# Performance work log

Measured on AMD Instinct MI355X. Metric: run time of the kernel, lower is better.

## Reference

```python
import jax, jax.numpy as jnp
import numpy as np

D = 1024; DI = 2048; HS = 16; PS = DI // HS; NS = 64; KC = 4; CHUNK = 64
HA = 16; HKV = 4; PA = D // HA; MLP_MULT = 4; ROPE_BASE = 10000.0
B_SZ = 2; L_SEQ = 2048


def rms_norm(x):
    eps = jnp.asarray(jnp.finfo(x.dtype).eps, x.dtype)
    return x * jax.lax.rsqrt(jnp.mean(jnp.square(x), axis=-1, keepdims=True) + eps)


def silu(x):
    return x * jax.nn.sigmoid(x)


def apply_rope(x, cos, sin):
    half = x.shape[-1] // 2
    x1, x2 = x[..., :half], x[..., half:]
    return jnp.concatenate([x1 * cos + x2 * sin, -x1 * sin + x2 * cos], axis=-1)


def selective_scan(x, A, Bm, Cm, dt, chunk):
    # x: [B,L,H,P], Bm/Cm: [B,L,H,N], A/dt: [H]. L must be a multiple of chunk.
    Bb, L, H, P = x.shape
    N = Bm.shape[-1]
    decay = jnp.exp(A * dt)  # [H]
    nc = L // chunk
    xp = x.reshape(Bb, nc, chunk, H, P).transpose(0, 1, 3, 2, 4)   # [B,nc,H,cs,P]
    Bp = Bm.reshape(Bb, nc, chunk, H, N).transpose(0, 1, 3, 2, 4)  # [B,nc,H,cs,N]
    Cp = Cm.reshape(Bb, nc, chunk, H, N).transpose(0, 1, 3, 2, 4)
    x_dt = xp * dt[None, None, :, None, None]
    idx = jnp.arange(chunk)
    diff = idx[:, None] - idx[None, :]
    # intra-chunk causal decay matrix L_mat: [H,cs,cs]
    Lm = jnp.where(diff >= 0, decay[:, None, None] ** jnp.maximum(diff, 0), 0.0)
    CB = jnp.einsum('bchqn,bchkn->bchqk', Cp, Bp)
    y_diag = jnp.einsum('bchqk,bchkp->bchqp', CB * Lm[None, None], x_dt)
    # per-chunk states
    decay_rev = decay[:, None] ** (chunk - 1 - idx)[None, :]  # [H,cs]
    states = jnp.einsum('bchtn,bchtp->bchnp', Bp * decay_rev[None, None, :, :, None], x_dt)
    # inter-chunk propagation
    ci = jnp.arange(nc)
    shift = ci[:, None] - ci[None, :] - 1
    cdec = decay ** chunk
    M = jnp.where(shift >= 0, cdec[:, None, None] ** jnp.maximum(shift, 0), 0.0)  # [H,nc,nc]
    h_carry = jnp.einsum('hij,bjhnp->bihnp', M, states)
    decay_out = decay[:, None] ** (idx + 1)[None, :]  # [H,cs]
    y_off = jnp.einsum('bchtn,bchnp->bchtp', Cp, h_carry) * decay_out[None, None, :, :, None]
    y = (y_diag + y_off).transpose(0, 1, 3, 2, 4).reshape(Bb, L, H, P)
    return y


def mlp(n, fc_w, proj_w):
    h = jax.nn.relu(n @ fc_w)
    return jnp.square(h) @ proj_w


def setup_inputs() -> dict:
    key = jax.random.key(0)
    ks = jax.random.split(key, 24)
    w = lambda k, shp, s=0.02: jax.random.normal(k, shp, jnp.float32) * s
    dt_init = jax.random.uniform(ks[0], (HS,), jnp.float32, 0.001, 0.1)
    dt_bias = dt_init + jnp.log(-jnp.expm1(-dt_init))  # inverse softplus
    return {
        'x': jax.random.normal(ks[1], (B_SZ, L_SEQ, D), jnp.float32),
        'in_proj_w': w(ks[2], (D, 2 * DI)),
        'conv_w': w(ks[3], (DI, KC), 0.2),
        'conv_b': jnp.zeros((DI,), jnp.float32),
        'B_proj_w': w(ks[4], (D, HS * NS)),
        'C_proj_w': w(ks[5], (D, HS * NS)),
        'dt_bias': dt_bias,
        'A_log': jnp.log(jnp.arange(1, HS + 1, dtype=jnp.float32)),
        'D_param': jnp.ones((HS,), jnp.float32),
        'out_proj_w': w(ks[6], (DI, D)),
        'resid_mix_m': jnp.stack([jnp.ones(D), jnp.zeros(D)]).astype(jnp.float32),
        'mamba_scale': jnp.ones((D,), jnp.float32),
        'm_fc_w': w(ks[7], (D, MLP_MULT * D)),
        'm_proj_w': w(ks[8], (MLP_MULT * D, D)),
        'm_mlp_scale': jnp.ones((D,), jnp.float32),
        'resid_mix_a': jnp.stack([jnp.ones(D), jnp.zeros(D)]).astype(jnp.float32),
        'q_w': w(ks[9], (D, D)),
        'k_w': w(ks[10], (D, HKV * PA)),
        'v_w': w(ks[11], (D, HKV * PA)),
        'o_w': w(ks[12], (D, D)),
        'q_gain': jnp.full((HA,), 1.0, jnp.float32),
        'attn_scale': jnp.ones((D,), jnp.float32),
        'a_fc_w': w(ks[13], (D, MLP_MULT * D)),
        'a_proj_w': w(ks[14], (MLP_MULT * D, D)),
        'a_mlp_scale': jnp.ones((D,), jnp.float32),
    }


def reference(x, in_proj_w, conv_w, conv_b, B_proj_w, C_proj_w, dt_bias, A_log, D_param, out_proj_w, resid_mix_m, mamba_scale, m_fc_w, m_proj_w, m_mlp_scale, resid_mix_a, q_w, k_w, v_w, o_w, q_gain, attn_scale, a_fc_w, a_proj_w, a_mlp_scale):
    Bb, L, _ = x.shape
    x0 = x
    # ---- Mamba block ----
    xm = resid_mix_m[0][None, None] * x + resid_mix_m[1][None, None] * x0
    n = rms_norm(xm)
    vg = n @ in_proj_w
    value, gate = vg[..., :DI], vg[..., DI:]
    v_t = value.transpose(0, 2, 1)  # [B, DI, L]
    v_conv = jax.lax.conv_general_dilated(
        v_t, conv_w[:, None, :], (1,), [(KC - 1, 0)],
        feature_group_count=DI, dimension_numbers=('NCH', 'OIH', 'NCH')) + conv_b[None, :, None]
    value = silu(v_conv).transpose(0, 2, 1).reshape(Bb, L, HS, PS)
    Bm = (xm @ B_proj_w).reshape(Bb, L, HS, NS)  # B/C use pre-norm (mixed) input
    Cm = (xm @ C_proj_w).reshape(Bb, L, HS, NS)
    dt = jax.nn.softplus(dt_bias)
    A = -jnp.exp(A_log)
    y = selective_scan(value, A, Bm, Cm, dt, CHUNK)
    y = y + D_param[None, None, :, None] * value
    y = (y.reshape(Bb, L, DI) * silu(gate)) @ out_proj_w
    xm = xm + mamba_scale[None, None] * y
    xm = xm + m_mlp_scale[None, None] * mlp(rms_norm(xm), m_fc_w, m_proj_w)
    # ---- Attention block ----
    xa = resid_mix_a[0][None, None] * xm + resid_mix_a[1][None, None] * x0
    n = rms_norm(xa)
    q = (n @ q_w).reshape(Bb, L, HA, PA).transpose(0, 2, 1, 3)
    k = (n @ k_w).reshape(Bb, L, HKV, PA).transpose(0, 2, 1, 3)
    v = (n @ v_w).reshape(Bb, L, HKV, PA).transpose(0, 2, 1, 3)
    q = rms_norm(q); k = rms_norm(k)
    inv_freq = 1.0 / (ROPE_BASE ** (jnp.arange(0, PA, 2, dtype=jnp.float32) / PA))
    f = jnp.outer(jnp.arange(L, dtype=jnp.float32), inv_freq)
    cos, sin = jnp.cos(f)[None, None], jnp.sin(f)[None, None]
    q = apply_rope(q, cos, sin) * q_gain[None, :, None, None]
    k = apply_rope(k, cos, sin)
    G = HA // HKV
    k = jnp.repeat(k, G, axis=1); v = jnp.repeat(v, G, axis=1)
    s = jnp.einsum('bhqd,bhkd->bhqk', q, k) / np.float32(np.sqrt(PA))
    mask = jnp.tril(jnp.ones((L, L), bool))
    s = jnp.where(mask[None, None], s, jnp.asarray(-jnp.inf, s.dtype))
    att = jax.nn.softmax(s, axis=-1)
    y = jnp.einsum('bhqk,bhkd->bhqd', att, v).transpose(0, 2, 1, 3).reshape(Bb, L, D)
    xa = xa + attn_scale[None, None] * (y @ o_w)
    xa = xa + a_mlp_scale[None, None] * mlp(rms_norm(xa), a_fc_w, a_proj_w)
    return xa
```

## Files before the change

### kernel.cpp

```cpp
#include <hip/hip_runtime.h>
#include <hip/hip_bf16.h>
#include <math.h>

#define D_ 1024
#define DI_ 2048
#define HS_ 16
#define PS_ 128
#define NS_ 64
#define HA_ 16
#define HKV_ 4
#define PA_ 64
#define B_ 2
#define L_ 2048
#define NT_ 4096
#define NC_ 32
#define RMS_EPS_ 1.1920929e-7f

typedef __attribute__((ext_vector_type(8))) short short8;
typedef __attribute__((ext_vector_type(4))) float f32x4;

#define GLOAD_LDS16(gp, lp)                                                        \
  __builtin_amdgcn_global_load_lds(                                               \
      (const __attribute__((address_space(1))) unsigned int*)(gp),                \
      (__attribute__((address_space(3))) unsigned int*)(lp), 16, 0, 0)

__global__ __launch_bounds__(256) void transpose_cvt(
    const float* __restrict__ W, __hip_bfloat16* __restrict__ Wt, int K, int N, int ldw) {
  __shared__ float t[32][33];
  int n0 = blockIdx.x * 32, k0 = blockIdx.y * 32;
  int tx = threadIdx.x & 31, ty = threadIdx.x >> 5;
#pragma unroll
  for (int i = 0; i < 4; i++)
    t[ty + i * 8][tx] = W[(size_t)(k0 + ty + i * 8) * ldw + n0 + tx];
  __syncthreads();
#pragma unroll
  for (int i = 0; i < 4; i++)
    Wt[(size_t)(n0 + ty + i * 8) * K + k0 + tx] = __float2bfloat16(t[tx][ty + i * 8]);
}

template<int BN>
__global__ __launch_bounds__(256) void gemm_bf16_t(
    const unsigned short* __restrict__ A, const unsigned short* __restrict__ Wt,
    float* __restrict__ Cf, __hip_bfloat16* __restrict__ Cb,
    const float* __restrict__ baseb, const float* __restrict__ scale,
    int N, int K, int gn, int mode) {
  constexpr int nWc = BN / 64;
  constexpr int nWr = 4 / nWc;
  constexpr int MF  = 8 / nWr;
  __shared__ unsigned short As[2][128 * 64];
  __shared__ unsigned short Bs[2][BN * 64];
  int lid = blockIdx.x;
  int x = lid & 7, r = lid >> 3;
  int RN = gn >> 2;
  int bm = ((x >> 2) * 16 + (r & 15)) * 128;
  int bn = ((x & 3) * RN + (r >> 4)) * BN;
  int tid = threadIdx.x;
  int w = tid >> 6, l = tid & 63;
  int wr = w / nWc, wc = w % nWc;
  int l15 = l & 15, lg = l >> 4;
  f32x4 acc[MF][4];
#pragma unroll
  for (int i = 0; i < MF; i++)
#pragma unroll
    for (int j = 0; j < 4; j++) acc[i][j] = (f32x4){0.f, 0.f, 0.f, 0.f};
  int r_ = tid >> 3;
  int s_ = tid & 7;

  auto STAGE = [&](int k0, int nb) {
#pragma unroll
    for (int i = 0; i < 4; i++) {
      int rr = i * 32 + r_;
      int kq = s_ ^ (rr & 7);
      GLOAD_LDS16(A + (size_t)(bm + rr) * K + k0 + kq * 8, &As[nb][rr * 64 + s_ * 8]);
    }
#pragma unroll
    for (int i = 0; i < BN / 32; i++) {
      int rr = i * 32 + r_;
      int kq = s_ ^ (rr & 7);
      GLOAD_LDS16(Wt + (size_t)(bn + rr) * K + k0 + kq * 8, &Bs[nb][rr * 64 + s_ * 8]);
    }
  };

  STAGE(0, 0);
  __syncthreads();
  int cur = 0;
  for (int k0 = 0; k0 < K; k0 += 64) {
    if (k0 + 64 < K) STAGE(k0 + 64, cur ^ 1);
#pragma unroll
    for (int h = 0; h < 2; h++) {
      short8 af[MF], bfr[4];
#pragma unroll
      for (int i = 0; i < MF; i++) {
        int row = wr * (16 * MF) + i * 16 + l15;
        int c = h * 4 + lg;
        af[i] = *(const short8*)&As[cur][row * 64 + ((c ^ (row & 7)) << 3)];
      }
#pragma unroll
      for (int j = 0; j < 4; j++) {
        int row = wc * 64 + j * 16 + l15;
        int c = h * 4 + lg;
        bfr[j] = *(const short8*)&Bs[cur][row * 64 + ((c ^ (row & 7)) << 3)];
      }
#pragma unroll
      for (int i = 0; i < MF; i++)
#pragma unroll
        for (int j = 0; j < 4; j++)
          acc[i][j] = __builtin_amdgcn_mfma_f32_16x16x32_bf16(af[i], bfr[j], acc[i][j], 0, 0, 0);
    }
    __syncthreads();
    cur ^= 1;
  }
  int rb = lg * 4, cb2 = l15;
#pragma unroll
  for (int i = 0; i < MF; i++)
#pragma unroll
    for (int j = 0; j < 4; j++) {
      int gr = bm + wr * (16 * MF) + i * 16 + rb;
      int gc = bn + wc * 64 + j * 16 + cb2;
#pragma unroll
      for (int reg = 0; reg < 4; reg++) {
        float v = acc[i][j][reg];
        size_t idx = (size_t)(gr + reg) * N + gc;
        if (mode == 0) {
          Cf[idx] = v;
        } else if (mode == 1) {
          v = fmaxf(v, 0.f);
          Cb[idx] = __float2bfloat16(v * v);
        } else if (mode == 2) {
          Cb[idx] = __float2bfloat16(v);
        } else {
          Cf[idx] = baseb[idx] + scale[gc] * v;
        }
      }
    }
}

__global__ __launch_bounds__(256) void mix_rms_kernel(
    const float* __restrict__ a, const float* __restrict__ b2,
    const float* __restrict__ mix, float* __restrict__ xout,
    __hip_bfloat16* __restrict__ nbf, __hip_bfloat16* __restrict__ rawbf) {
  int row = blockIdx.x;
  size_t base = (size_t)row * D_;
  float v[4]; float ss = 0.f;
#pragma unroll
  for (int i = 0; i < 4; i++) {
    int d = threadIdx.x + i * 256;
    float val = mix[d] * a[base + d] + mix[D_ + d] * b2[base + d];
    v[i] = val; ss += val * val;
  }
  for (int o = 32; o > 0; o >>= 1) ss += __shfl_down(ss, o, 64);
  __shared__ float red[4];
  if ((threadIdx.x & 63) == 0) red[threadIdx.x >> 6] = ss;
  __syncthreads();
  float inv = rsqrtf((red[0] + red[1] + red[2] + red[3]) * (1.f / D_) + RMS_EPS_);
#pragma unroll
  for (int i = 0; i < 4; i++) {
    int d = threadIdx.x + i * 256;
    xout[base + d] = v[i];
    nbf[base + d] = __float2bfloat16(v[i] * inv);
    if (rawbf) rawbf[base + d] = __float2bfloat16(v[i]);
  }
}

__global__ __launch_bounds__(256) void rms_kernel(
    const float* __restrict__ a, __hip_bfloat16* __restrict__ nbf) {
  int row = blockIdx.x;
  size_t base = (size_t)row * D_;
  float v[4]; float ss = 0.f;
#pragma unroll
  for (int i = 0; i < 4; i++) {
    int d = threadIdx.x + i * 256;
    float val = a[base + d];
    v[i] = val; ss += val * val;
  }
  for (int o = 32; o > 0; o >>= 1) ss += __shfl_down(ss, o, 64);
  __shared__ float red[4];
  if ((threadIdx.x & 63) == 0) red[threadIdx.x >> 6] = ss;
  __syncthreads();
  float inv = rsqrtf((red[0] + red[1] + red[2] + red[3]) * (1.f / D_) + RMS_EPS_);
#pragma unroll
  for (int i = 0; i < 4; i++) {
    int d = threadIdx.x + i * 256;
    nbf[base + d] = __float2bfloat16(v[i] * inv);
  }
}

__global__ __launch_bounds__(256) void conv_silu_kernel(
    const __hip_bfloat16* __restrict__ vg, const float* __restrict__ cw,
    const float* __restrict__ cb, float* __restrict__ xv) {
  int idx = blockIdx.x * 256 + threadIdx.x;
  int c = idx & (DI_ - 1);
  int bl = idx >> 11;
  int l = bl & (L_ - 1);
  float acc = cb[c];
  float w0 = cw[c * 4 + 0], w1 = cw[c * 4 + 1], w2 = cw[c * 4 + 2], w3 = cw[c * 4 + 3];
  size_t rb = (size_t)bl * 4096 + c;
  if (l >= 3) acc += __bfloat162float(vg[rb - (size_t)3 * 4096]) * w0;
  if (l >= 2) acc += __bfloat162float(vg[rb - (size_t)2 * 4096]) * w1;
  if (l >= 1) acc += __bfloat162float(vg[rb - (size_t)1 * 4096]) * w2;
  acc += __bfloat162float(vg[rb]) * w3;
  xv[idx] = acc / (1.f + __expf(-acc));
}

__global__ __launch_bounds__(256) void scanA1_kernel(
    const float* __restrict__ xv, const __hip_bfloat16* __restrict__ BCm,
    const float* __restrict__ dt_bias, const float* __restrict__ A_log,
    float* __restrict__ st) {
  __shared__ __align__(16) float sm[4096 + 8192];
  float* Bs = sm;
  float* Xs = sm + 4096;
  int blk = blockIdx.x;
  int c = blk & 31, h = (blk >> 5) & 15, b = blk >> 9;
  float dt = log1pf(__expf(dt_bias[h]));
  float adt = -__expf(A_log[h]) * dt;
  int tid = threadIdx.x;
  int l0 = c * 64;
  size_t rB = ((size_t)(b * L_ + l0)) * 2048 + h * NS_;
#pragma unroll
  for (int i = 0; i < 16; i++) {
    int e = tid + i * 256;
    int t = e >> 6, n = e & 63;
    Bs[t * 64 + n] = __bfloat162float(BCm[rB + (size_t)t * 2048 + n]);
  }
  size_t rX = ((size_t)(b * L_ + l0)) * DI_ + h * PS_;
#pragma unroll
  for (int i = 0; i < 32; i++) {
    int e = tid + i * 256;
    int t = e >> 7, p = e & 127;
    Xs[t * 128 + p] = xv[rX + (size_t)t * DI_ + p];
  }
  __syncthreads();
  int pg = tid & 31;
  int ng = (tid >> 5) << 3;
  float acc[8][4];
#pragma unroll
  for (int nn = 0; nn < 8; nn++)
#pragma unroll
    for (int i = 0; i < 4; i++) acc[nn][i] = 0.f;
  for (int t = 0; t < 64; t++) {
    float dr = __expf(adt * (float)(63 - t));
    float4 x4 = *(const float4*)&Xs[t * 128 + pg * 4];
    float xd0 = x4.x * dr, xd1 = x4.y * dr, xd2 = x4.z * dr, xd3 = x4.w * dr;
#pragma unroll
    for (int nn = 0; nn < 8; nn++) {
      float bv = Bs[t * 64 + ng + nn];
      acc[nn][0] += bv * xd0; acc[nn][1] += bv * xd1;
      acc[nn][2] += bv * xd2; acc[nn][3] += bv * xd3;
    }
  }
  size_t sb = ((size_t)((b * HS_ + h) * NC_ + c)) * (NS_ * PS_);
#pragma unroll
  for (int nn = 0; nn < 8; nn++) {
    *(float4*)&st[sb + (size_t)(ng + nn) * PS_ + pg * 4] =
        make_float4(acc[nn][0] * dt, acc[nn][1] * dt, acc[nn][2] * dt, acc[nn][3] * dt);
  }
}

__global__ __launch_bounds__(256) void scanA2_kernel(
    const float* __restrict__ xv, const __hip_bfloat16* __restrict__ BCm,
    const float* __restrict__ dt_bias,
    const float* __restrict__ A_log, const float* __restrict__ D_param,
    float* __restrict__ y) {
  __shared__ __align__(16) float sm[4160 + 8192];
  float* Cb = sm;
  float* Bs = sm + 4160;
  float* Xs = sm + 4160;
  int blk = blockIdx.x;
  int c = blk & 31, h = (blk >> 5) & 15, b = blk >> 9;
  float dt = log1pf(__expf(dt_bias[h]));
  float adt = -__expf(A_log[h]) * dt;
  float Dp = D_param[h];
  int tid = threadIdx.x;
  int l0 = c * 64;
  size_t rB = ((size_t)(b * L_ + l0)) * 2048 + h * NS_;
#pragma unroll
  for (int i = 0; i < 16; i++) {
    int e = tid + i * 256;
    int t = e >> 6, n = e & 63;
    Bs[t * 64 + n] = __bfloat162float(BCm[rB + (size_t)t * 2048 + n]);
    Cb[t * 65 + n] = __bfloat162float(BCm[rB + 1024 + (size_t)t * 2048 + n]);
  }
  __syncthreads();
  int q = tid >> 2;
  int kb = (tid & 3) << 4;
  float cbl[16];
#pragma unroll
  for (int kk = 0; kk < 16; kk++) {
    int k = kb + kk;
    float a = 0.f;
    if (k <= q) {
      for (int n = 0; n < 64; n++) a += Cb[q * 65 + n] * Bs[k * 64 + n];
      a *= __expf(adt * (float)(q - k));
    }
    cbl[kk] = a;
  }
  __syncthreads();
#pragma unroll
  for (int kk = 0; kk < 16; kk++) Cb[q * 65 + kb + kk] = cbl[kk];
  size_t rX = ((size_t)(b * L_ + l0)) * DI_ + h * PS_;
#pragma unroll
  for (int i = 0; i < 32; i++) {
    int e = tid + i * 256;
    int t = e >> 7, p = e & 127;
    Xs[t * 128 + p] = xv[rX + (size_t)t * DI_ + p];
  }
  __syncthreads();
  int pg = tid & 31;
  int qg = (tid >> 5) << 3;
  float acc[8][4];
#pragma unroll
  for (int qq = 0; qq < 8; qq++)
#pragma unroll
    for (int i = 0; i < 4; i++) acc[qq][i] = 0.f;
  for (int k = 0; k < 64; k++) {
    float4 x4 = *(const float4*)&Xs[k * 128 + pg * 4];
#pragma unroll
    for (int qq = 0; qq < 8; qq++) {
      float s = Cb[(qg + qq) * 65 + k];
      acc[qq][0] += s * x4.x; acc[qq][1] += s * x4.y;
      acc[qq][2] += s * x4.z; acc[qq][3] += s * x4.w;
    }
  }
#pragma unroll
  for (int qq = 0; qq < 8; qq++) {
    int qr = qg + qq;
    float4 xq = *(const float4*)&Xs[qr * 128 + pg * 4];
    size_t yo = ((size_t)(b * L_ + l0 + qr)) * DI_ + h * PS_ + pg * 4;
    *(float4*)&y[yo] = make_float4(acc[qq][0] * dt + Dp * xq.x,
                                   acc[qq][1] * dt + Dp * xq.y,
                                   acc[qq][2] * dt + Dp * xq.z,
                                   acc[qq][3] * dt + Dp * xq.w);
  }
}

__global__ __launch_bounds__(256) void scanB1_kernel(
    float* __restrict__ st, const float* __restrict__ dt_bias,
    const float* __restrict__ A_log) {
  int slice = blockIdx.x & 3;
  int h = (blockIdx.x >> 2) & 15, b = blockIdx.x >> 6;
  float dt = log1pf(__expf(dt_bias[h]));
  float adt = -__expf(A_log[h]) * dt;
  float cdec = __expf(adt * 64.f);
  size_t base = ((size_t)(b * HS_ + h)) * NC_ * (NS_ * PS_) + slice * 2048 + threadIdx.x;
  float hreg[8];
#pragma unroll
  for (int j = 0; j < 8; j++) hreg[j] = 0.f;
  for (int c = 0; c < NC_; c++) {
    size_t o = base + (size_t)c * (NS_ * PS_);
#pragma unroll
    for (int j = 0; j < 8; j++) {
      float tmp = st[o + (size_t)j * 256];
      st[o + (size_t)j * 256] = hreg[j];
      hreg[j] = cdec * hreg[j] + tmp;
    }
  }
}

__global__ __launch_bounds__(256) void scanB2_kernel(
    const __hip_bfloat16* __restrict__ BCm, const float* __restrict__ st,
    const __hip_bfloat16* __restrict__ vg, const float* __restrict__ dt_bias,
    const float* __restrict__ A_log, const float* __restrict__ y,
    __hip_bfloat16* __restrict__ yout) {
  __shared__ float Cs[64 * 64];
  __shared__ __align__(16) float Hs[64 * 128];
  int blk = blockIdx.x;
  int c = blk & 31, h = (blk >> 5) & 15, b = blk >> 9;
  float dt = log1pf(__expf(dt_bias[h]));
  float adt = -__expf(A_log[h]) * dt;
  int tid = threadIdx.x;
  int l0 = c * 64;
  size_t rC = ((size_t)(b * L_ + l0)) * 2048 + 1024 + h * NS_;
#pragma unroll
  for (int i = 0; i < 16; i++) {
    int e = tid + i * 256;
    int t = e >> 6, n = e & 63;
    Cs[t * 64 + n] = __bfloat162float(BCm[rC + (size_t)t * 2048 + n]);
  }
  size_t sb = ((size_t)((b * HS_ + h) * NC_ + c)) * (NS_ * PS_);
#pragma unroll
  for (int i = 0; i < 32; i++) {
    int e = tid + i * 256;
    Hs[e] = st[sb + e];
  }
  __syncthreads();
  int pg = tid & 31;
  int tg = (tid >> 5) << 3;
  float acc[8][4];
#pragma unroll
  for (int tt = 0; tt < 8; tt++)
#pragma unroll
    for (int i = 0; i < 4; i++) acc[tt][i] = 0.f;
  for (int n = 0; n < 64; n++) {
    float4 h4 = *(const float4*)&Hs[n * 128 + pg * 4];
#pragma unroll
    for (int tt = 0; tt < 8; tt++) {
      float cv = Cs[(tg + tt) * 64 + n];
      acc[tt][0] += cv * h4.x; acc[tt][1] += cv * h4.y;
      acc[tt][2] += cv * h4.z; acc[tt][3] += cv * h4.w;
    }
  }
#pragma unroll
  for (int tt = 0; tt < 8; tt++) {
    int t = tg + tt;
    float dout = __expf(adt * (float)(t + 1));
    size_t row = (size_t)(b * L_ + l0 + t);
#pragma unroll
    for (int i = 0; i < 4; i++) {
      int p = pg * 4 + i;
      float g = __bfloat162float(vg[row * 4096 + 2048 + h * PS_ + p]);
      float yv = y[row * DI_ + h * PS_ + p] + acc[tt][i] * dout;
      yout[row * DI_ + h * PS_ + p] = __float2bfloat16(yv * (g / (1.f + __expf(-g))));
    }
  }
}

__global__ void rope_fill_kernel(float* __restrict__ cosb, float* __restrict__ sinb) {
  int idx = blockIdx.x * 256 + threadIdx.x;
  int i = idx & 31, l = idx >> 5;
  float inv = __expf(-(2.0f * (float)i / (float)PA_) * logf(10000.0f));
  float ang = (float)l * inv;
  cosb[idx] = cosf(ang);
  sinb[idx] = sinf(ang);
}

__global__ __launch_bounds__(256) void qknorm_rope_bf16_kernel(
    const float* __restrict__ src, int srcstride, int srcofs,
    __hip_bfloat16* __restrict__ dst, int nh,
    const float* __restrict__ cosb, const float* __restrict__ sinb,
    const float* __restrict__ gain) {
  int row = blockIdx.x * 4 + (threadIdx.x >> 6);
  int lane = threadIdx.x & 63;
  int h = row % nh;
  int tok = row / nh;
  int l = tok & (L_ - 1);
  float v = src[(size_t)tok * srcstride + srcofs + h * 64 + lane];
  float ss = v * v;
  for (int o = 32; o > 0; o >>= 1) ss += __shfl_xor(ss, o, 64);
  v *= rsqrtf(ss * (1.f / PA_) + RMS_EPS_);
  float partner = __shfl_xor(v, 32, 64);
  int i = lane & 31;
  float cth = cosb[l * 32 + i], sth = sinb[l * 32 + i];
  float out = (lane < 32) ? (v * cth + partner * sth) : (v * cth - partner * sth);
  if (gain) out *= gain[h];
  dst[(size_t)tok * (nh * 64) + h * 64 + lane] = __float2bfloat16(out);
}

__global__ __launch_bounds__(256) void attn_mfma_kernel(
    const unsigned short* __restrict__ qb, const unsigned short* __restrict__ kb,
    const unsigned short* __restrict__ vt, const float* __restrict__ qgain,
    __hip_bfloat16* __restrict__ ao) {
  __shared__ unsigned short Ks[64][72];
  __shared__ unsigned short Vs[64][72];
  __shared__ unsigned short Psm[4][16][72];
  int blk = blockIdx.x;
  int qi = blk & 15;
  int h  = (blk >> 4) & 15;
  int b  = blk >> 8;
  int hk = h >> 2;
  int tid = threadIdx.x;
  int w = tid >> 6, l = tid & 63;
  int l15 = l & 15, lg = l >> 4;
  int r0 = tid >> 3, s0 = tid & 7;
  float mstat = 8.0f * fabsf(qgain[h]);
  const unsigned short* kbase = kb + (size_t)b * L_ * (HKV_ * PA_) + hk * PA_ + s0 * 8;
  const unsigned short* vbase = vt + ((size_t)(b * HKV_ + hk) * PA_) * L_ + s0 * 8;

  for (int pass = 0; pass < 2; pass++) {
    int qt = pass ? (31 - qi) : qi;
    int q0 = qt * 64;
    int qw = q0 + w * 16;
    short8 qf[2];
    {
      size_t qrow = ((size_t)(b * L_ + qw + l15)) * (HA_ * PA_) + h * PA_;
      qf[0] = *(const short8*)&qb[qrow + lg * 8];
      qf[1] = *(const short8*)&qb[qrow + 32 + lg * 8];
    }
    f32x4 o_acc[4];
#pragma unroll
    for (int db = 0; db < 4; db++) o_acc[db] = (f32x4){0.f, 0.f, 0.f, 0.f};
    f32x4 lsum = (f32x4){0.f, 0.f, 0.f, 0.f};
    int nkt = qt + 1;
    short8 kr0 = *(const short8*)&kbase[(size_t)r0 * (HKV_ * PA_)];
    short8 kr1 = *(const short8*)&kbase[(size_t)(r0 + 32) * (HKV_ * PA_)];
    short8 vr0 = *(const short8*)&vbase[(size_t)r0 * L_];
    short8 vr1 = *(const short8*)&vbase[(size_t)(r0 + 32) * L_];
    for (int kt = 0; kt < nkt; kt++) {
      int k0 = kt * 64;
      __syncthreads();
      *(short8*)&Ks[r0][s0 * 8] = kr0;
      *(short8*)&Ks[r0 + 32][s0 * 8] = kr1;
      *(short8*)&Vs[r0][s0 * 8] = vr0;
      *(short8*)&Vs[r0 + 32][s0 * 8] = vr1;
      if (kt + 1 < nkt) {
        int k1 = k0 + 64;
        kr0 = *(const short8*)&kbase[(size_t)(k1 + r0) * (HKV_ * PA_)];
        kr1 = *(const short8*)&kbase[(size_t)(k1 + r0 + 32) * (HKV_ * PA_)];
        vr0 = *(const short8*)&vbase[(size_t)r0 * L_ + k1];
        vr1 = *(const short8*)&vbase[(size_t)(r0 + 32) * L_ + k1];
      }
      __syncthreads();
      f32x4 s_acc[4];
#pragma unroll
      for (int kb2 = 0; kb2 < 4; kb2++) {
        short8 b0 = *(const short8*)&Ks[kb2 * 16 + l15][lg * 8];
        short8 b1 = *(const short8*)&Ks[kb2 * 16 + l15][32 + lg * 8];
        f32x4 s = (f32x4){0.f, 0.f, 0.f, 0.f};
        s = __builtin_amdgcn_mfma_f32_16x16x32_bf16(qf[0], b0, s, 0, 0, 0);
        s = __builtin_amdgcn_mfma_f32_16x16x32_bf16(qf[1], b1, s, 0, 0, 0);
        s_acc[kb2] = s;
      }
      bool diag = (kt == qt);
#pragma unroll
      for (int kb2 = 0; kb2 < 4; kb2++) {
        int key = k0 + kb2 * 16 + l15;
#pragma unroll
        for (int reg = 0; reg < 4; reg++) {
          float p = __expf(s_acc[kb2][reg] * 0.125f - mstat);
          if (diag && key > qw + lg * 4 + reg) p = 0.f;
          lsum[reg] += p;
          __hip_bfloat16 hv = __float2bfloat16(p);
          Psm[w][lg * 4 + reg][kb2 * 16 + l15] = *(unsigned short*)&hv;
        }
      }
      asm volatile("s_waitcnt lgkmcnt(0)" ::: "memory");
#pragma unroll
      for (int ks = 0; ks < 2; ks++) {
        short8 pa = *(const short8*)&Psm[w][l15][ks * 32 + lg * 8];
#pragma unroll
        for (int db = 0; db < 4; db++) {
          short8 vb8 = *(const short8*)&Vs[db * 16 + l15][ks * 32 + lg * 8];
          o_acc[db] = __builtin_amdgcn_mfma_f32_16x16x32_bf16(pa, vb8, o_acc[db], 0, 0, 0);
        }
      }
    }
#pragma unroll
    for (int of = 1; of < 16; of <<= 1) {
      lsum[0] += __shfl_xor(lsum[0], of, 64);
      lsum[1] += __shfl_xor(lsum[1], of, 64);
      lsum[2] += __shfl_xor(lsum[2], of, 64);
      lsum[3] += __shfl_xor(lsum[3], of, 64);
    }
#pragma unroll
    for (int reg = 0; reg < 4; reg++) {
      float invl = 1.0f / lsum[reg];
      size_t row = (size_t)(b * L_ + qw + lg * 4 + reg);
#pragma unroll
      for (int db = 0; db < 4; db++)
        ao[row * D_ + h * PA_ + db * 16 + l15] = __float2bfloat16(o_acc[db][reg] * invl);
    }
  }
}

extern "C" void kernel_launch(void* const* d_in, const int* in_sizes, int n_in,
                              void* d_out, int out_size, void* d_ws, size_t ws_size,
                              hipStream_t stream) {
  (void)in_sizes; (void)n_in; (void)out_size; (void)ws_size;
  const float* x           = (const float*)d_in[0];
  const float* in_proj_w   = (const float*)d_in[1];
  const float* conv_w      = (const float*)d_in[2];
  const float* conv_b      = (const float*)d_in[3];
  const float* B_proj_w    = (const float*)d_in[4];
  const float* C_proj_w    = (const float*)d_in[5];
  const float* dt_bias     = (const float*)d_in[6];
  const float* A_log       = (const float*)d_in[7];
  const float* D_param     = (const float*)d_in[8];
  const float* out_proj_w  = (const float*)d_in[9];
  const float* resid_mix_m = (const float*)d_in[10];
  const float* mamba_scale = (const float*)d_in[11];
  const float* m_fc_w      = (const float*)d_in[12];
  const float* m_proj_w    = (const float*)d_in[13];
  const float* m_mlp_scale = (const float*)d_in[14];
  const float* resid_mix_a = (const float*)d_in[15];
  const float* q_w         = (const float*)d_in[16];
  const float* k_w         = (const float*)d_in[17];
  const float* v_w         = (const float*)d_in[18];
  const float* o_w         = (const float*)d_in[19];
  const float* q_gain      = (const float*)d_in[20];
  const float* attn_scale  = (const float*)d_in[21];
  const float* a_fc_w      = (const float*)d_in[22];
  const float* a_proj_w    = (const float*)d_in[23];
  const float* a_mlp_scale = (const float*)d_in[24];
  float* ws  = (float*)d_ws;
  float* out = (float*)d_out;

  float* xm    = ws;
  float* vgR   = ws + 4194304;
  float* xvR   = ws + 12582912;
  float* stR   = ws + 20971520;
  float* nbR   = ws + 29360128;
  float* xmbR  = ws + 31457280;
  float* BCR   = ws + 33554432;
  float* WtR   = ws + 37748736;
  float* cosb  = ws + 51642368;
  float* sinb  = cosb + 65536;

  __hip_bfloat16* vg  = (__hip_bfloat16*)vgR;
  float*          qkvf = vgR;
  float*          xv  = xvR;
  float*          st  = stR;
  __hip_bfloat16* hb  = (__hip_bfloat16*)stR;
  __hip_bfloat16* nbb = (__hip_bfloat16*)nbR;
  __hip_bfloat16* xmb = (__hip_bfloat16*)xmbR;
  __hip_bfloat16* ybb = (__hip_bfloat16*)nbR;
  __hip_bfloat16* BCm = (__hip_bfloat16*)BCR;
  __hip_bfloat16* qbb = (__hip_bfloat16*)xvR;
  __hip_bfloat16* kbb = (__hip_bfloat16*)(xvR + 2097152);
  __hip_bfloat16* vtb = (__hip_bfloat16*)(xvR + 2621440);
  __hip_bfloat16* aob = (__hip_bfloat16*)(xvR + 3145728);

  __hip_bfloat16* Wt = (__hip_bfloat16*)WtR;
  size_t o_in  = 0;
  size_t o_B   = o_in  + (size_t)4096 * 1024;
  size_t o_out = o_B   + (size_t)2048 * 1024;
  size_t o_mfc = o_out + (size_t)1024 * 2048;
  size_t o_mpj = o_mfc + (size_t)4096 * 1024;
  size_t o_qkv = o_mpj + (size_t)1024 * 4096;
  size_t o_o   = o_qkv + (size_t)1536 * 1024;
  size_t o_afc = o_o   + (size_t)1024 * 1024;
  size_t o_apj = o_afc + (size_t)4096 * 1024;

#define TCVT(Wp, off, K, N) \
  transpose_cvt<<<dim3((N) / 32, (K) / 32), 256, 0, stream>>>((Wp), Wt + (off), (K), (N), (N))
  TCVT(in_proj_w,  o_in,  1024, 4096);
  TCVT(B_proj_w,   o_B,   1024, 1024);
  TCVT(C_proj_w,   o_B + (size_t)1024 * 1024, 1024, 1024);
  TCVT(out_proj_w, o_out, 2048, 1024);
  TCVT(m_fc_w,     o_mfc, 1024, 4096);
  TCVT(m_proj_w,   o_mpj, 4096, 1024);
  TCVT(q_w,        o_qkv, 1024, 1024);
  TCVT(k_w,        o_qkv + (size_t)1024 * 1024, 1024, 256);
  TCVT(v_w,        o_qkv + (size_t)1280 * 1024, 1024, 256);
  TCVT(o_w,        o_o,   1024, 1024);
  TCVT(a_fc_w,     o_afc, 1024, 4096);
  TCVT(a_proj_w,   o_apj, 4096, 1024);
#undef TCVT

#define GEMM(BN, Abuf, Woff, Cfp, Cbp, basep, scalep, N, K, mode) \
  gemm_bf16_t<BN><<<32 * ((N) / (BN)), 256, 0, stream>>>( \
      (const unsigned short*)(Abuf), (const unsigned short*)(Wt + (Woff)), \
      (Cfp), (Cbp), (basep), (scalep), (N), (K), (N) / (BN), (mode))

  mix_rms_kernel<<<NT_, 256, 0, stream>>>(x, x, resid_mix_m, xm, nbb, xmb);
  GEMM(128, nbb, o_in, (float*)0, vg, (const float*)0, (const float*)0, 4096, 1024, 2);
  GEMM(128, xmb, o_B, (float*)0, BCm, (const float*)0, (const float*)0, 2048, 1024, 2);
  conv_silu_kernel<<<NT_ * DI_ / 256, 256, 0, stream>>>(vg, conv_w, conv_b, xv);
  scanA1_kernel<<<B_ * HS_ * NC_, 256, 0, stream>>>(xv, BCm, dt_bias, A_log, st);
  scanA2_kernel<<<B_ * HS_ * NC_, 256, 0, stream>>>(xv, BCm, dt_bias, A_log, D_param, xv);
  scanB1_kernel<<<B_ * HS_ * 4, 256, 0, stream>>>(st, dt_bias, A_log);
  scanB2_kernel<<<B_ * HS_ * NC_, 256, 0, stream>>>(BCm, st, vg, dt_bias, A_log, xv, ybb);
  GEMM(64, ybb, o_out, xm, (__hip_bfloat16*)0, xm, mamba_scale, 1024, 2048, 3);
  rms_kernel<<<NT_, 256, 0, stream>>>(xm, nbb);
  GEMM(128, nbb, o_mfc, (float*)0, hb, (const float*)0, (const float*)0, 4096, 1024, 1);
  GEMM(64, hb, o_mpj, xm, (__hip_bfloat16*)0, xm, m_mlp_scale, 1024, 4096, 3);
  mix_rms_kernel<<<NT_, 256, 0, stream>>>(xm, x, resid_mix_a, xm, nbb, (__hip_bfloat16*)0);
  GEMM(64, nbb, o_qkv, qkvf, (__hip_bfloat16*)0, (const float*)0, (const float*)0, 1536, 1024, 0);
  rope_fill_kernel<<<L_ * 32 / 256, 256, 0, stream>>>(cosb, sinb);
  qknorm_rope_bf16_kernel<<<NT_ * HA_ / 4, 256, 0, stream>>>(qkvf, 1536, 0, qbb, HA_, cosb, sinb, q_gain);
  qknorm_rope_bf16_kernel<<<NT_ * HKV_ / 4, 256, 0, stream>>>(qkvf, 1536, 1024, kbb, HKV_, cosb, sinb, (const float*)0);
  transpose_cvt<<<dim3(256 / 32, 2048 / 32), 256, 0, stream>>>(qkvf + 1280, vtb, 2048, 256, 1536);
  transpose_cvt<<<dim3(256 / 32, 2048 / 32), 256, 0, stream>>>(qkvf + (size_t)L_ * 1536 + 1280, vtb + (size_t)256 * L_, 2048, 256, 1536);
  attn_mfma_kernel<<<B_ * HA_ * 16, 256, 0, stream>>>(
      (const unsigned short*)qbb, (const unsigned short*)kbb, (const unsigned short*)vtb,
      q_gain, aob);
  GEMM(64, aob, o_o, xm, (__hip_bfloat16*)0, xm, attn_scale, 1024, 1024, 3);
  rms_kernel<<<NT_, 256, 0, stream>>>(xm, nbb);
  GEMM(128, nbb, o_afc, (float*)0, hb, (const float*)0, (const float*)0, 4096, 1024, 1);
  GEMM(64, hb, o_apj, out, (__hip_bfloat16*)0, xm, a_mlp_scale, 1024, 4096, 3);
#undef GEMM
}
```

Baseline: 708.7 us.

## Add 256x256-tile triple-buffered GEMM for the 4096-wide projections

Adds a 512-thread GEMM kernel with 256x256 output tiles, K-step 32, three LDS buffers filled by direct global-to-LDS loads, and an XOR-swizzled layout. It is used for the in_proj and the two MLP fc GEMMs, which have N=4096 and K=1024. Larger tiles raise arithmetic intensity and cut redundant operand loads, and the triple buffering overlaps loads with MFMA. The cost is a grid of only 256 blocks, higher register use (128 accumulator floats per thread), and hardcoded N and K. Mode 2 does no activation, so in_proj output stays the same.

Measured after the change: 680.6 us. 1.04x faster.

```diff
diff --git a/kernel.cpp b/kernel.cpp
--- a/kernel.cpp
+++ b/kernel.cpp
@@ -36,6 +36,84 @@
 #pragma unroll
   for (int i = 0; i < 4; i++)
     Wt[(size_t)(n0 + ty + i * 8) * K + k0 + tx] = __float2bfloat16(t[tx][ty + i * 8]);
+}
+
+template<int MODE>
+__global__ __launch_bounds__(512) void gemm256_k32(
+    const unsigned short* __restrict__ A, const unsigned short* __restrict__ Wt,
+    __hip_bfloat16* __restrict__ Cb, int N, int K) {
+  __shared__ unsigned short As[3][256 * 32];
+  __shared__ unsigned short Bs[3][256 * 32];
+  int lid = blockIdx.x;
+  int x = lid & 7, r = lid >> 3;
+  int bm = ((x >> 2) * 8 + (r & 7)) * 256;
+  int bn = ((x & 3) * 4 + (r >> 3)) * 256;
+  int tid = threadIdx.x;
+  int w = tid >> 6, l = tid & 63;
+  int wr = w >> 2, wc = w & 3;
+  int l15 = l & 15, lg = l >> 4;
+  int rr = tid >> 2, ss = tid & 3;
+
+  f32x4 acc[8][4];
+#pragma unroll
+  for (int i = 0; i < 8; i++)
+#pragma unroll
+    for (int j = 0; j < 4; j++) acc[i][j] = (f32x4){0.f, 0.f, 0.f, 0.f};
+
+  auto STAGE = [&](int kt, int nb) {
+    int k0 = kt * 32;
+#pragma unroll
+    for (int p = 0; p < 2; p++) {
+      int row = p * 128 + rr;
+      int kq = ss ^ ((row >> 1) & 3);
+      GLOAD_LDS16(A + (size_t)(bm + row) * K + k0 + kq * 8, &As[nb][row * 32 + ss * 8]);
+    }
+#pragma unroll
+    for (int p = 0; p < 2; p++) {
+      int row = p * 128 + rr;
+      int kq = ss ^ ((row >> 1) & 3);
+      GLOAD_LDS16(Wt + (size_t)(bn + row) * K + k0 + kq * 8, &Bs[nb][row * 32 + ss * 8]);
+    }
+  };
+
+  int KT = K >> 5;
+  STAGE(0, 0);
+  STAGE(1, 1);
+  int buf = 0;
+  for (int t = 0; t < KT; ++t) {
+    asm volatile("s_waitcnt vmcnt(4)" ::: "memory");
+    __builtin_amdgcn_s_barrier();
+    __builtin_amdgcn_sched_barrier(0);
+    if (t + 2 < KT) STAGE(t + 2, (t + 2) % 3);
+    short8 bf[4];
+#pragma unroll
+    for (int j = 0; j < 4; j++) {
+      int row = wc * 64 + j * 16 + l15;
+      bf[j] = *(const short8*)&Bs[buf][row * 32 + ((lg ^ ((row >> 1) & 3)) << 3)];
+    }
+#pragma unroll
+    for (int i = 0; i < 8; i++) {
+      int row = wr * 128 + i * 16 + l15;
+      short8 af = *(const short8*)&As[buf][row * 32 + ((lg ^ ((row >> 1) & 3)) << 3)];
+#pragma unroll
+      for (int j = 0; j < 4; j++)
+        acc[i][j] = __builtin_amdgcn_mfma_f32_16x16x32_bf16(af, bf[j], acc[i][j], 0, 0, 0);
+    }
+    buf = (buf + 1) % 3;
+  }
+#pragma unroll
+  for (int i = 0; i < 8; i++)
+#pragma unroll
+    for (int j = 0; j < 4; j++) {
+      int gr = bm + wr * 128 + i * 16 + lg * 4;
+      int gc = bn + wc * 64 + j * 16 + l15;
+#pragma unroll
+      for (int reg = 0; reg < 4; reg++) {
+        float v = acc[i][j][reg];
+        if (MODE == 1) { v = fmaxf(v, 0.f); v = v * v; }
+        Cb[(size_t)(gr + reg) * N + gc] = __float2bfloat16(v);
+      }
+    }
 }
 
 template<int BN>
@@ -639,9 +717,13 @@
   gemm_bf16_t<BN><<<32 * ((N) / (BN)), 256, 0, stream>>>( \
       (const unsigned short*)(Abuf), (const unsigned short*)(Wt + (Woff)), \
       (Cfp), (Cbp), (basep), (scalep), (N), (K), (N) / (BN), (mode))
+#define GEMM256(MODE, Abuf, Woff, Cbp) \
+  gemm256_k32<MODE><<<256, 512, 0, stream>>>( \
+      (const unsigned short*)(Abuf), (const unsigned short*)(Wt + (Woff)), \
+      (Cbp), 4096, 1024)
 
   mix_rms_kernel<<<NT_, 256, 0, stream>>>(x, x, resid_mix_m, xm, nbb, xmb);
-  GEMM(128, nbb, o_in, (float*)0, vg, (const float*)0, (const float*)0, 4096, 1024, 2);
+  GEMM256(2, nbb, o_in, vg);
   GEMM(128, xmb, o_B, (float*)0, BCm, (const float*)0, (const float*)0, 2048, 1024, 2);
   conv_silu_kernel<<<NT_ * DI_ / 256, 256, 0, stream>>>(vg, conv_w, conv_b, xv);
   scanA1_kernel<<<B_ * HS_ * NC_, 256, 0, stream>>>(xv, BCm, dt_bias, A_log, st);
@@ -650,7 +732,7 @@
   scanB2_kernel<<<B_ * HS_ * NC_, 256, 0, stream>>>(BCm, st, vg, dt_bias, A_log, xv, ybb);
   GEMM(64, ybb, o_out, xm, (__hip_bfloat16*)0, xm, mamba_scale, 1024, 2048, 3);
   rms_kernel<<<NT_, 256, 0, stream>>>(xm, nbb);
-  GEMM(128, nbb, o_mfc, (float*)0, hb, (const float*)0, (const float*)0, 4096, 1024, 1);
+  GEMM256(1, nbb, o_mfc, hb);
   GEMM(64, hb, o_mpj, xm, (__hip_bfloat16*)0, xm, m_mlp_scale, 1024, 4096, 3);
   mix_rms_kernel<<<NT_, 256, 0, stream>>>(xm, x, resid_mix_a, xm, nbb, (__hip_bfloat16*)0);
   GEMM(64, nbb, o_qkv, qkvf, (__hip_bfloat16*)0, (const float*)0, (const float*)0, 1536, 1024, 0);
@@ -664,7 +746,8 @@
       q_gain, aob);
   GEMM(64, aob, o_o, xm, (__hip_bfloat16*)0, xm, attn_scale, 1024, 1024, 3);
   rms_kernel<<<NT_, 256, 0, stream>>>(xm, nbb);
-  GEMM(128, nbb, o_afc, (float*)0, hb, (const float*)0, (const float*)0, 4096, 1024, 1);
+  GEMM256(1, nbb, o_afc, hb);
   GEMM(64, hb, o_apj, out, (__hip_bfloat16*)0, xm, a_mlp_scale, 1024, 4096, 3);
 #undef GEMM
-}
+#undef GEMM256
+}
```
